# Kernel tuning notes

Hardware: AMD Instinct MI355X
Metric: run time of the kernel (lower is better)

## Reference

```python
import jax, jax.numpy as jnp
import numpy as np

B, S, D, H, HD = 2, 4096, 768, 12, 64
W = 256  # one-sided attention window (attention_window=512 // 2)
SCALE = 1.0 / np.sqrt(HD).astype(np.float32)
NEG = -1e9


def setup_inputs() -> dict:
    key = jax.random.key(0)
    ks = jax.random.split(key, 13)
    inp = {"hidden_states": jax.random.normal(ks[0], (B, S, D), dtype=jnp.float32)}
    names = ["Wq", "Wk", "Wv", "Wqg", "Wkg", "Wvg"]
    for i, n in enumerate(names):
        inp[n] = jax.random.normal(ks[1 + i], (D, D), dtype=jnp.float32) * 0.02
        inp["b" + n[1:]] = jax.random.normal(ks[7 + i], (D,), dtype=jnp.float32) * 0.02
    inp["num_global"] = 32
    return inp


def _heads(x):
    # [B,S,D] -> [B,H,S,HD]
    return x.reshape(B, S, H, HD).transpose(0, 2, 1, 3)


def longformer_attn(hidden_states, Wq, bq, Wk, bk, Wv, bv, Wqg, bqg, Wkg, bkg, Wvg, bvg, G):
    q = _heads(hidden_states @ Wq + bq) * SCALE
    k = _heads(hidden_states @ Wk + bk)
    v = _heads(hidden_states @ Wv + bv)

    nc = S // W  # number of query chunks
    # --- banded (sliding window) scores via overlapping key chunks of size 3W ---
    Qc = q.reshape(B, H, nc, W, HD)
    kpad = jnp.pad(k, ((0, 0), (0, 0), (W, W), (0, 0)))
    win_idx = jnp.arange(nc)[:, None] * W + jnp.arange(3 * W)[None, :]  # [nc, 3W]
    K3 = kpad[:, :, win_idx]  # [B,H,nc,3W,HD]
    band = jnp.einsum('bhcqd,bhckd->bhcqk', Qc, K3)  # [B,H,nc,W,3W]
    # mask: key abs position in range, and relative offset within [-W, W]
    c = jnp.arange(nc)[:, None, None]
    pq = jnp.arange(W)[None, :, None]
    e = jnp.arange(3 * W)[None, None, :]
    kabs = c * W + e - W
    valid = (kabs >= 0) & (kabs < S) & (e >= pq) & (e <= pq + 2 * W)
    band = jnp.where(valid[None, None], band, NEG).reshape(B, H, S, 3 * W)

    # --- all queries also attend to the G global keys (regular key proj) ---
    sg = jnp.einsum('bhsd,bhgd->bhsg', q, k[:, :, :G])  # [B,H,S,G]
    probs = jax.nn.softmax(jnp.concatenate([sg, band], axis=-1), axis=-1)
    pg, pb = probs[..., :G], probs[..., G:].reshape(B, H, nc, W, 3 * W)

    vpad = jnp.pad(v, ((0, 0), (0, 0), (W, W), (0, 0)))
    V3 = vpad[:, :, win_idx]  # [B,H,nc,3W,HD]
    out = jnp.einsum('bhcqk,bhckd->bhcqd', pb, V3).reshape(B, H, S, HD)
    out = out + jnp.einsum('bhsg,bhgd->bhsd', pg, v[:, :, :G])

    # --- global queries attend to ALL tokens with the *_global projections ---
    qg = _heads(hidden_states @ Wqg + bqg)[:, :, :G] * SCALE  # [B,H,G,HD]
    kgf = _heads(hidden_states @ Wkg + bkg)
    vgf = _heads(hidden_states @ Wvg + bvg)
    gp = jax.nn.softmax(jnp.einsum('bhgd,bhsd->bhgs', qg, kgf), axis=-1)
    gout = jnp.einsum('bhgs,bhsd->bhgd', gp, vgf)  # [B,H,G,HD]
    out = out.at[:, :, :G].set(gout)

    return out.transpose(0, 2, 1, 3).reshape(B, S, D)


def reference(hidden_states, Wq, bq, Wk, bk, Wv, bv, Wqg, bqg, Wkg, bkg, Wvg, bvg, num_global):
    return longformer_attn(hidden_states, Wq, bq, Wk, bk, Wv, bv, Wqg, bqg, Wkg, bkg, Wvg, bvg, int(num_global))
```

## Files before the change

### kernel.cpp

```cpp
#include <hip/hip_runtime.h>
#include <hip/hip_bf16.h>


#define DEVI __device__ __forceinline__
typedef _Float16 f16;
typedef _Float16 h4 __attribute__((ext_vector_type(4)));
typedef _Float16 f16x8 __attribute__((ext_vector_type(8)));
typedef __attribute__((ext_vector_type(4))) float float4v;

DEVI float4v mfma16(f16x8 a, f16x8 b, float4v c) {
    return __builtin_amdgcn_mfma_f32_16x16x32_f16(a, b, c, 0, 0, 0);
}

DEVI void gl_lds16(const f16* g, f16* l) {
    __builtin_amdgcn_global_load_lds(
        (const __attribute__((address_space(1))) unsigned int*)g,
        (__attribute__((address_space(3))) unsigned int*)l, 16, 0, 0);
}

__global__ __launch_bounds__(256) void prep(
    const float* __restrict__ x,
    const float* __restrict__ w0, const float* __restrict__ w1,
    const float* __restrict__ w2, const float* __restrict__ w3,
    const float* __restrict__ w4, const float* __restrict__ w5,
    f16* __restrict__ xh, f16* __restrict__ wt) {
    __shared__ float tile[64][65];
    int bid = blockIdx.x;
    if (bid < 6144) {
        int i = (bid * 256 + threadIdx.x) * 4;
        float4 v = *(const float4*)&x[i];
        h4 o = {(f16)v.x, (f16)v.y, (f16)v.z, (f16)v.w};
        *(h4*)&xh[i] = o;
    } else {
        int t = bid - 6144;
        int i = t / 144, rem = t - i * 144;
        int n0 = (rem % 12) * 64, k0 = (rem / 12) * 64;
        const float* W = (i == 0) ? w0 : (i == 1) ? w1 : (i == 2) ? w2
                       : (i == 3) ? w3 : (i == 4) ? w4 : w5;
        int tx = threadIdx.x & 63, ty = threadIdx.x >> 6;
#pragma unroll
        for (int yy = 0; yy < 64; yy += 4)
            tile[yy + ty][tx] = W[(size_t)(k0 + yy + ty) * 768 + n0 + tx];
        __syncthreads();
#pragma unroll
        for (int yy = 0; yy < 64; yy += 4)
            wt[(size_t)(i * 768 + n0 + yy + ty) * 768 + k0 + tx] = (f16)tile[tx][yy + ty];
    }
}

__global__ __launch_bounds__(256, 2) void qkv_mfma11(
    const f16* __restrict__ Xh, const f16* __restrict__ Wt,
    const float* __restrict__ b0, const float* __restrict__ b1,
    const float* __restrict__ b2, const float* __restrict__ b3,
    const float* __restrict__ b4, const float* __restrict__ b5,
    f16* __restrict__ q, f16* __restrict__ k, f16* __restrict__ vT,
    f16* __restrict__ qg, f16* __restrict__ kg, f16* __restrict__ vgT) {
    __shared__ __align__(16) char smem[73728];
    f16* As = (f16*)smem;
    f16* Bs = (f16*)(smem + 24576);
    f16* Cl = (f16*)smem;

    int tid = threadIdx.x, lane = tid & 63, wid = tid >> 6;
    int quad = lane >> 4, l15 = lane & 15;

    int L = blockIdx.x + (blockIdx.y << 6);
    int xcd = L & 7, W = L >> 3;
    int mt = xcd * 8 + (W & 7);
    int yy = W >> 3;
    int m0 = mt * 128;
    int grp = yy / 3;
    if (grp == 3 && (m0 & 4095) != 0) return;
    int nb = (yy - grp * 3) * 256;
    int wm = (wid >> 1) * 64;
    int wn = (wid & 1) * 128;
    const f16* arow0 = Xh + (size_t)m0 * 768;
    const f16* brow0 = Wt + (size_t)(grp * 768 + nb) * 768;

    float4v acc[4][8];
#pragma unroll
    for (int i = 0; i < 4; ++i)
#pragma unroll
        for (int j = 0; j < 8; ++j) acc[i][j] = (float4v){0.f, 0.f, 0.f, 0.f};

    int r0 = tid >> 2;
    int o0 = (((tid & 3) ^ ((r0 >> 1) & 3)) << 3);
    int sw8 = ((quad ^ ((l15 >> 1) & 3)) << 3);

    auto STAGE_T = [&](int kt, int buf) {
        int k0 = kt << 5;
        const f16* ag = &arow0[(size_t)r0 * 768 + k0 + o0];
        const f16* bg = &brow0[(size_t)r0 * 768 + k0 + o0];
        f16* al = As + buf * 4096 + wid * 512;
        f16* bl = Bs + buf * 8192 + wid * 512;
        gl_lds16(ag, al);
        gl_lds16(ag + (size_t)64 * 768, al + 2048);
        gl_lds16(bg, bl);
        gl_lds16(bg + (size_t)64 * 768, bl + 2048);
        gl_lds16(bg + (size_t)128 * 768, bl + 4096);
        gl_lds16(bg + (size_t)192 * 768, bl + 6144);
    };

    auto COMPUTE_T = [&](int t) {
        const f16* Ab = As + (t % 3) * 4096;
        const f16* Bb = Bs + (t % 3) * 8192;
        f16x8 af[4], bf[8];
#pragma unroll
        for (int i = 0; i < 4; ++i)
            af[i] = *(const f16x8*)&Ab[(wm + i * 16 + l15) * 32 + sw8];
#pragma unroll
        for (int j = 0; j < 8; ++j)
            bf[j] = *(const f16x8*)&Bb[(wn + j * 16 + l15) * 32 + sw8];
        __builtin_amdgcn_s_setprio(1);
#pragma unroll
        for (int i = 0; i < 4; ++i)
#pragma unroll
            for (int j = 0; j < 8; ++j)
                acc[i][j] = mfma16(af[i], bf[j], acc[i][j]);
        __builtin_amdgcn_s_setprio(0);
    };

    STAGE_T(0, 0);
    STAGE_T(1, 1);
#pragma unroll
    for (int t = 0; t < 24; ++t) {
        if (t < 23) {
            asm volatile("s_waitcnt vmcnt(6)" ::: "memory");
        } else {
            asm volatile("s_waitcnt vmcnt(0)" ::: "memory");
        }
        __builtin_amdgcn_s_barrier();
        __builtin_amdgcn_sched_barrier(0);
        if (t + 2 <= 23) STAGE_T(t + 2, (t + 2) % 3);
        COMPUTE_T(t);
    }
    __syncthreads();

    const float* Bsel = (grp == 0) ? b0 : (grp == 1) ? b1 : (grp == 2) ? b2
                      : (grp == 3) ? b3 : (grp == 4) ? b4 : b5;
    int b = m0 >> 12;
    bool tr = (grp == 2 || grp == 5);

    if (tr) {
        constexpr int CLD2 = 136;
#pragma unroll
        for (int j = 0; j < 8; ++j) {
            float bias = Bsel[nb + wn + j * 16 + l15];
#pragma unroll
            for (int i = 0; i < 4; ++i) {
                float4v a = acc[i][j];
                h4 pk = {(f16)(a[0] + bias), (f16)(a[1] + bias),
                         (f16)(a[2] + bias), (f16)(a[3] + bias)};
                *(h4*)&Cl[(wn + j * 16 + l15) * CLD2 + wm + i * 16 + quad * 4] = pk;
            }
        }
        __syncthreads();
        f16* base = (grp == 2) ? vT : vgT;
        int c = tid;
        int ncol = nb + c, h = ncol >> 6, hd = ncol & 63;
        f16* dst = &base[((size_t)((b * 12 + h) * 64 + hd)) * 4096 + (m0 & 4095)];
        const f16* src = &Cl[c * CLD2];
#pragma unroll
        for (int ii = 0; ii < 16; ++ii)
            *(f16x8*)&dst[ii * 8] = *(const f16x8*)&src[ii * 8];
    } else {
        constexpr int CLD = 264;
        float scale = (grp == 0 || grp == 3) ? 0.125f : 1.0f;
#pragma unroll
        for (int j = 0; j < 8; ++j) {
            float bias = Bsel[nb + wn + j * 16 + l15];
#pragma unroll
            for (int i = 0; i < 4; ++i) {
                float4v a = acc[i][j];
#pragma unroll
                for (int r = 0; r < 4; ++r)
                    Cl[(wm + i * 16 + quad * 4 + r) * CLD + wn + j * 16 + l15] =
                        (f16)((a[r] + bias) * scale);
            }
        }
        __syncthreads();
        int row = tid & 127, half = tid >> 7;
        int s = (m0 & 4095) + row;
        const f16* src = &Cl[row * CLD + half * 128];
        if (grp == 3) {
            if (s < 32) {
#pragma unroll
                for (int ii = 0; ii < 16; ++ii) {
                    int h = (nb >> 6) + (half << 1) + (ii >> 3), hd = (ii & 7) * 8;
                    *(f16x8*)&qg[((size_t)((b * 12 + h) * 32 + s)) * 64 + hd] =
                        *(const f16x8*)&src[ii * 8];
                }
            }
        } else {
            f16* baseb = (grp == 0) ? q : (grp == 1) ? k : kg;
#pragma unroll
            for (int ii = 0; ii < 16; ++ii) {
                int h = (nb >> 6) + (half << 1) + (ii >> 3), hd = (ii & 7) * 8;
                *(f16x8*)&baseb[((size_t)((b * 12 + h) * 4096 + s)) * 64 + hd] =
                    *(const f16x8*)&src[ii * 8];
            }
        }
    }
}

__global__ __launch_bounds__(256, 3) void band_global(
    const f16* __restrict__ q, const f16* __restrict__ k, const f16* __restrict__ vT,
    const f16* __restrict__ qg, const f16* __restrict__ kg, const f16* __restrict__ vgT,
    float* __restrict__ out, float* __restrict__ Opart, float* __restrict__ Lpart) {
    __shared__ __align__(16) char smem[51712];
    int tid = threadIdx.x, lane = tid & 63, wid = tid >> 6;
    int quad = lane >> 4, l15 = lane & 15;

    if (blockIdx.x < 768) {
        constexpr int LDK = 72, LDV = 136, LDP = 40;
        f16* Kt = (f16*)smem;
        f16* Vt = (f16*)(smem + 18432);
        f16* PW = (f16*)(smem + 35840) + wid * 32 * LDP;
        int c = blockIdx.x & 31, h = (blockIdx.x >> 5) % 12, b = blockIdx.x / 384;
        const f16* qsl = q + (size_t)(b * 12 + h) * 4096 * 64;
        const f16* ksl = k + (size_t)(b * 12 + h) * 4096 * 64;
        const f16* vsl = vT + (size_t)(b * 12 + h) * 64 * 4096;
        int q0 = c * 128;
        int pq0 = q0 + wid * 32;

        f16x8 qf[2][2];
#pragma unroll
        for (int qg2 = 0; qg2 < 2; ++qg2)
#pragma unroll
            for (int ks = 0; ks < 2; ++ks)
                qf[qg2][ks] = *(const f16x8*)&qsl[(size_t)(pq0 + qg2 * 16 + l15) * 64 +
                                                  ks * 32 + quad * 8];

        float4v Ot[4][2];
#pragma unroll
        for (int dt = 0; dt < 4; ++dt)
#pragma unroll
            for (int qg2 = 0; qg2 < 2; ++qg2) Ot[dt][qg2] = (float4v){0.f, 0.f, 0.f, 0.f};
        float lacc[2] = {0.f, 0.f};

        {
#pragma unroll
            for (int jt = 0; jt < 2; ++jt) {
                f16x8 kf0 = *(const f16x8*)&ksl[(size_t)(jt * 16 + l15) * 64 + quad * 8];
                f16x8 kf1 = *(const f16x8*)&ksl[(size_t)(jt * 16 + l15) * 64 + 32 + quad * 8];
#pragma unroll
                for (int qg2 = 0; qg2 < 2; ++qg2) {
                    float4v sacc = (float4v){0.f, 0.f, 0.f, 0.f};
                    sacc = mfma16(kf0, qf[qg2][0], sacc);
                    sacc = mfma16(kf1, qf[qg2][1], sacc);
                    float p0 = __expf(sacc[0]), p1 = __expf(sacc[1]);
                    float p2 = __expf(sacc[2]), p3 = __expf(sacc[3]);
                    lacc[qg2] += (p0 + p1) + (p2 + p3);
                    h4 pk = {(f16)p0, (f16)p1, (f16)p2, (f16)p3};
                    *(h4*)&PW[(qg2 * 16 + l15) * LDP + jt * 16 + quad * 4] = pk;
                }
            }
            f16x8 pf0 = *(const f16x8*)&PW[l15 * LDP + quad * 8];
            f16x8 pf1 = *(const f16x8*)&PW[(16 + l15) * LDP + quad * 8];
#pragma unroll
            for (int dt = 0; dt < 4; ++dt) {
                f16x8 vf = *(const f16x8*)&vsl[(size_t)(dt * 16 + l15) * 4096 + quad * 8];
                Ot[dt][0] = mfma16(vf, pf0, Ot[dt][0]);
                Ot[dt][1] = mfma16(vf, pf1, Ot[dt][1]);
            }
        }

        for (int r = 0; r < 5; ++r) {
            int kb = q0 - 256 + r * 128;
            if (kb < 0 || kb >= 4096) continue;
            __syncthreads();
            {
                int kr = tid >> 1, ko = (tid & 1) * 32;
                const f16* ks2 = &ksl[(size_t)(kb + kr) * 64 + ko];
                f16* kd = &Kt[kr * LDK + ko];
#pragma unroll
                for (int i = 0; i < 4; ++i) *(f16x8*)&kd[i * 8] = *(const f16x8*)&ks2[i * 8];
                int vr = tid >> 2, vo = (tid & 3) * 32;
                const f16* vs2 = &vsl[(size_t)vr * 4096 + kb + vo];
                f16* vd = &Vt[vr * LDV + vo];
#pragma unroll
                for (int i = 0; i < 4; ++i) *(f16x8*)&vd[i * 8] = *(const f16x8*)&vs2[i * 8];
            }
            __syncthreads();

            if (kb + 127 < pq0 - 256 || kb > pq0 + 287) continue;

#pragma unroll
            for (int tt = 0; tt < 2; ++tt) {
                int tb = kb + tt * 64;
                if (tb + 63 < pq0 - 256 || tb > pq0 + 287) continue;
#pragma unroll
                for (int hf = 0; hf < 2; ++hf) {
#pragma unroll
                    for (int jt = 0; jt < 2; ++jt) {
                        int jl = tt * 64 + hf * 32 + jt * 16;
                        f16x8 kf0 = *(const f16x8*)&Kt[(jl + l15) * LDK + quad * 8];
                        f16x8 kf1 = *(const f16x8*)&Kt[(jl + l15) * LDK + 32 + quad * 8];
                        int j0 = kb + jl;
#pragma unroll
                        for (int qg2 = 0; qg2 < 2; ++qg2) {
                            int qlo = pq0 + qg2 * 16;
                            h4 pk = {(f16)0.f, (f16)0.f, (f16)0.f, (f16)0.f};
                            bool dead = (j0 < qlo - 271) || (j0 > qlo + 271);
                            if (!dead) {
                                float4v sacc = (float4v){0.f, 0.f, 0.f, 0.f};
                                sacc = mfma16(kf0, qf[qg2][0], sacc);
                                sacc = mfma16(kf1, qf[qg2][1], sacc);
                                float p[4];
                                bool full = (j0 >= qlo - 241) && (j0 <= qlo + 241);
                                if (full) {
#pragma unroll
                                    for (int rr = 0; rr < 4; ++rr) p[rr] = __expf(sacc[rr]);
                                } else {
#pragma unroll
                                    for (int rr = 0; rr < 4; ++rr) {
                                        int d = (j0 + quad * 4 + rr) - (qlo + l15);
                                        p[rr] = ((unsigned)(d + 256) <= 512u) ? __expf(sacc[rr]) : 0.f;
                                    }
                                }
                                lacc[qg2] += (p[0] + p[1]) + (p[2] + p[3]);
                                pk = (h4){(f16)p[0], (f16)p[1], (f16)p[2], (f16)p[3]};
                            }
                            *(h4*)&PW[(qg2 * 16 + l15) * LDP + jt * 16 + quad * 4] = pk;
                        }
                    }
                    f16x8 pf0 = *(const f16x8*)&PW[l15 * LDP + quad * 8];
                    f16x8 pf1 = *(const f16x8*)&PW[(16 + l15) * LDP + quad * 8];
#pragma unroll
                    for (int dt = 0; dt < 4; ++dt) {
                        f16x8 vf = *(const f16x8*)&Vt[(dt * 16 + l15) * LDV +
                                                      tt * 64 + hf * 32 + quad * 8];
                        Ot[dt][0] = mfma16(vf, pf0, Ot[dt][0]);
                        Ot[dt][1] = mfma16(vf, pf1, Ot[dt][1]);
                    }
                }
            }
        }

#pragma unroll
        for (int qg2 = 0; qg2 < 2; ++qg2) {
            float lsum = lacc[qg2];
            lsum += __shfl_xor(lsum, 16);
            lsum += __shfl_xor(lsum, 32);
            float inv = 1.f / lsum;
            size_t orow = (size_t)(b * 4096 + pq0 + qg2 * 16 + l15) * 768 + h * 64;
#pragma unroll
            for (int dt = 0; dt < 4; ++dt) {
                float4 o4 = {Ot[dt][qg2][0] * inv, Ot[dt][qg2][1] * inv,
                             Ot[dt][qg2][2] * inv, Ot[dt][qg2][3] * inv};
                *(float4*)&out[orow + dt * 16 + quad * 4] = o4;
            }
        }
    } else {
        constexpr int LDP = 72;
        f16* PW = (f16*)smem + wid * 32 * LDP;
        float* Osh = (float*)(smem + 18432);
        float* Lsh = (float*)(smem + 18432 + 32768);
        int bid = blockIdx.x - 768;
        int sl = bid & 7, bh = bid >> 3;
        const f16* qsl = qg + (size_t)bh * 32 * 64;
        const f16* ksl = kg + (size_t)bh * 4096 * 64;
        const f16* vsl = vgT + (size_t)bh * 64 * 4096;
        int kbase = sl * 512 + wid * 128;

        f16x8 qf[2][2];
#pragma unroll
        for (int g = 0; g < 2; ++g)
#pragma unroll
            for (int ks = 0; ks < 2; ++ks)
                qf[g][ks] = *(const f16x8*)&qsl[(size_t)(g * 16 + l15) * 64 + ks * 32 + quad * 8];

        float4v Ot[4][2];
#pragma unroll
        for (int dt = 0; dt < 4; ++dt)
#pragma unroll
            for (int g = 0; g < 2; ++g) Ot[dt][g] = (float4v){0.f, 0.f, 0.f, 0.f};
        float lacc[2] = {0.f, 0.f};

#pragma unroll
        for (int hf = 0; hf < 2; ++hf) {
            int kh0 = kbase + hf * 64;
#pragma unroll
            for (int kt = 0; kt < 4; ++kt) {
                int jb = kh0 + kt * 16;
                f16x8 kf0 = *(const f16x8*)&ksl[(size_t)(jb + l15) * 64 + quad * 8];
                f16x8 kf1 = *(const f16x8*)&ksl[(size_t)(jb + l15) * 64 + 32 + quad * 8];
#pragma unroll
                for (int g = 0; g < 2; ++g) {
                    float4v sacc = (float4v){0.f, 0.f, 0.f, 0.f};
                    sacc = mfma16(kf0, qf[g][0], sacc);
                    sacc = mfma16(kf1, qf[g][1], sacc);
                    float p0 = __expf(sacc[0]), p1 = __expf(sacc[1]);
                    float p2 = __expf(sacc[2]), p3 = __expf(sacc[3]);
                    lacc[g] += (p0 + p1) + (p2 + p3);
                    h4 pk = {(f16)p0, (f16)p1, (f16)p2, (f16)p3};
                    *(h4*)&PW[(g * 16 + l15) * LDP + kt * 16 + quad * 4] = pk;
                }
            }
#pragma unroll
            for (int kh = 0; kh < 2; ++kh) {
                f16x8 pf0 = *(const f16x8*)&PW[l15 * LDP + kh * 32 + quad * 8];
                f16x8 pf1 = *(const f16x8*)&PW[(16 + l15) * LDP + kh * 32 + quad * 8];
#pragma unroll
                for (int dt = 0; dt < 4; ++dt) {
                    f16x8 vf = *(const f16x8*)&vsl[(size_t)(dt * 16 + l15) * 4096 +
                                                   kh0 + kh * 32 + quad * 8];
                    Ot[dt][0] = mfma16(vf, pf0, Ot[dt][0]);
                    Ot[dt][1] = mfma16(vf, pf1, Ot[dt][1]);
                }
            }
        }

#pragma unroll
        for (int g = 0; g < 2; ++g) {
            lacc[g] += __shfl_xor(lacc[g], 16);
            lacc[g] += __shfl_xor(lacc[g], 32);
        }
        if (quad == 0) { Lsh[wid * 32 + l15] = lacc[0]; Lsh[wid * 32 + 16 + l15] = lacc[1]; }
#pragma unroll
        for (int dt = 0; dt < 4; ++dt)
#pragma unroll
            for (int g = 0; g < 2; ++g)
#pragma unroll
                for (int r = 0; r < 4; ++r)
                    Osh[wid * 2048 + (dt * 16 + quad * 4 + r) * 32 + g * 16 + l15] = Ot[dt][g][r];
        __syncthreads();
#pragma unroll
        for (int i = 0; i < 8; ++i) {
            int idx = tid + i * 256;
            int d = idx & 63, qq = idx >> 6;
            float v = Osh[0 * 2048 + d * 32 + qq] + Osh[1 * 2048 + d * 32 + qq] +
                      Osh[2 * 2048 + d * 32 + qq] + Osh[3 * 2048 + d * 32 + qq];
            Opart[(size_t)bid * 2048 + idx] = v;
        }
        if (tid < 32)
            Lpart[bid * 32 + tid] = Lsh[0 * 32 + tid] + Lsh[1 * 32 + tid] +
                                    Lsh[2 * 32 + tid] + Lsh[3 * 32 + tid];
    }
}

__global__ __launch_bounds__(256) void global_reduce(
    const float* __restrict__ Opart, const float* __restrict__ Lpart,
    float* __restrict__ out) {
    __shared__ float Ls[32];
    int tid = threadIdx.x, bh = blockIdx.x;
    int b = bh / 12, h = bh % 12;
    if (tid < 32) {
        float s = 0.f;
#pragma unroll
        for (int sl = 0; sl < 8; ++sl) s += Lpart[(bh * 8 + sl) * 32 + tid];
        Ls[tid] = s;
    }
    __syncthreads();
#pragma unroll
    for (int i = 0; i < 8; ++i) {
        int idx = tid + i * 256;
        int d = idx & 63, qq = idx >> 6;
        float o = 0.f;
#pragma unroll
        for (int sl = 0; sl < 8; ++sl) o += Opart[(size_t)(bh * 8 + sl) * 2048 + idx];
        out[(size_t)(b * 4096 + qq) * 768 + h * 64 + d] = o / Ls[qq];
    }
}

extern "C" void kernel_launch(void* const* d_in, const int* in_sizes, int n_in,
                              void* d_out, int out_size, void* d_ws, size_t ws_size,
                              hipStream_t stream) {
    const float* hs = (const float*)d_in[0];
    float* outp = (float*)d_out;

    char* p = (char*)d_ws;
    const size_t SLAB = (size_t)2 * 12 * 4096 * 64 * sizeof(f16);
    f16* qb   = (f16*)(p + 0 * SLAB);
    f16* kb   = (f16*)(p + 1 * SLAB);
    f16* vtb  = (f16*)(p + 2 * SLAB);
    f16* kgb  = (f16*)(p + 3 * SLAB);
    f16* vgtb = (f16*)(p + 4 * SLAB);
    f16* qgb  = (f16*)(p + 5 * SLAB);
    char* p2  = p + 5 * SLAB + 196608;
    f16* xh   = (f16*)p2;
    f16* wt   = (f16*)(p2 + SLAB);
    char* p3  = p2 + SLAB + 7077888;
    float* Opart = (float*)p3;
    float* Lpart = (float*)(p3 + 1572864);

    prep<<<7008, 256, 0, stream>>>(
        hs,
        (const float*)d_in[1], (const float*)d_in[3], (const float*)d_in[5],
        (const float*)d_in[7], (const float*)d_in[9], (const float*)d_in[11],
        xh, wt);
    qkv_mfma11<<<dim3(64, 18), 256, 0, stream>>>(
        xh, wt,
        (const float*)d_in[2], (const float*)d_in[4], (const float*)d_in[6],
        (const float*)d_in[8], (const float*)d_in[10], (const float*)d_in[12],
        qb, kb, vtb, qgb, kgb, vgtb);
    band_global<<<960, 256, 0, stream>>>(
        qb, kb, vtb, qgb, kgb, vgtb, outp, Opart, Lpart);
    global_reduce<<<24, 256, 0, stream>>>(Opart, Lpart, outp);
}
```

Before: 220.8 us.

## Fuse global-query attention reduction into band kernel, drop separate reduce launch

The global-query attention for each (batch, head) now runs in a single block that loops over all 4096 keys and normalizes the result in place, instead of 192 split-K blocks that wrote partials to a separate reduction kernel. These 24 long blocks are scheduled first in the merged grid. Band blocks now skip writing the first 32 rows, which the global blocks own. This removes one kernel launch, the partial-buffer traffic and a redundant band write. The cost is less parallelism: each global block does eight times more sequential work and may become the tail of the launch.

After: 239.3 us, median of 2. 8.4% more time.

```diff
diff --git a/kernel.cpp b/kernel.cpp
--- a/kernel.cpp
+++ b/kernel.cpp
@@ -202,20 +202,107 @@
     }
 }
 
-__global__ __launch_bounds__(256, 3) void band_global(
+__global__ __launch_bounds__(256, 3) void band_global2(
     const f16* __restrict__ q, const f16* __restrict__ k, const f16* __restrict__ vT,
     const f16* __restrict__ qg, const f16* __restrict__ kg, const f16* __restrict__ vgT,
-    float* __restrict__ out, float* __restrict__ Opart, float* __restrict__ Lpart) {
+    float* __restrict__ out) {
     __shared__ __align__(16) char smem[51712];
     int tid = threadIdx.x, lane = tid & 63, wid = tid >> 6;
     int quad = lane >> 4, l15 = lane & 15;
 
-    if (blockIdx.x < 768) {
+    if (blockIdx.x < 24) {
+        constexpr int LDP = 72;
+        f16* PW = (f16*)smem + wid * 32 * LDP;
+        float* Osh = (float*)(smem + 18432);
+        float* Lsh = (float*)(smem + 18432 + 32768);
+        int bh = blockIdx.x;
+        int h = bh % 12, b = bh / 12;
+        const f16* qsl = qg + (size_t)bh * 32 * 64;
+        const f16* ksl = kg + (size_t)bh * 4096 * 64;
+        const f16* vsl = vgT + (size_t)bh * 64 * 4096;
+
+        f16x8 qf[2][2];
+#pragma unroll
+        for (int g = 0; g < 2; ++g)
+#pragma unroll
+            for (int ks = 0; ks < 2; ++ks)
+                qf[g][ks] = *(const f16x8*)&qsl[(size_t)(g * 16 + l15) * 64 + ks * 32 + quad * 8];
+
+        float4v Ot[4][2];
+#pragma unroll
+        for (int dt = 0; dt < 4; ++dt)
+#pragma unroll
+            for (int g = 0; g < 2; ++g) Ot[dt][g] = (float4v){0.f, 0.f, 0.f, 0.f};
+        float lacc[2] = {0.f, 0.f};
+
+        for (int it = 0; it < 8; ++it) {
+            int kbase = wid * 1024 + it * 128;
+#pragma unroll
+            for (int hf = 0; hf < 2; ++hf) {
+                int kh0 = kbase + hf * 64;
+#pragma unroll
+                for (int kt = 0; kt < 4; ++kt) {
+                    int jb = kh0 + kt * 16;
+                    f16x8 kf0 = *(const f16x8*)&ksl[(size_t)(jb + l15) * 64 + quad * 8];
+                    f16x8 kf1 = *(const f16x8*)&ksl[(size_t)(jb + l15) * 64 + 32 + quad * 8];
+#pragma unroll
+                    for (int g = 0; g < 2; ++g) {
+                        float4v sacc = (float4v){0.f, 0.f, 0.f, 0.f};
+                        sacc = mfma16(kf0, qf[g][0], sacc);
+                        sacc = mfma16(kf1, qf[g][1], sacc);
+                        float p0 = __expf(sacc[0]), p1 = __expf(sacc[1]);
+                        float p2 = __expf(sacc[2]), p3 = __expf(sacc[3]);
+                        lacc[g] += (p0 + p1) + (p2 + p3);
+                        h4 pk = {(f16)p0, (f16)p1, (f16)p2, (f16)p3};
+                        *(h4*)&PW[(g * 16 + l15) * LDP + kt * 16 + quad * 4] = pk;
+                    }
+                }
+#pragma unroll
+                for (int kh = 0; kh < 2; ++kh) {
+                    f16x8 pf0 = *(const f16x8*)&PW[l15 * LDP + kh * 32 + quad * 8];
+                    f16x8 pf1 = *(const f16x8*)&PW[(16 + l15) * LDP + kh * 32 + quad * 8];
+#pragma unroll
+                    for (int dt = 0; dt < 4; ++dt) {
+                        f16x8 vf = *(const f16x8*)&vsl[(size_t)(dt * 16 + l15) * 4096 +
+                                                       kh0 + kh * 32 + quad * 8];
+                        Ot[dt][0] = mfma16(vf, pf0, Ot[dt][0]);
+                        Ot[dt][1] = mfma16(vf, pf1, Ot[dt][1]);
+                    }
+                }
+            }
+        }
+
+#pragma unroll
+        for (int g = 0; g < 2; ++g) {
+            lacc[g] += __shfl_xor(lacc[g], 16);
+            lacc[g] += __shfl_xor(lacc[g], 32);
+        }
+        if (quad == 0) { Lsh[wid * 32 + l15] = lacc[0]; Lsh[wid * 32 + 16 + l15] = lacc[1]; }
+#pragma unroll
+        for (int dt = 0; dt < 4; ++dt)
+#pragma unroll
+            for (int g = 0; g < 2; ++g)
+#pragma unroll
+                for (int r = 0; r < 4; ++r)
+                    Osh[wid * 2048 + (dt * 16 + quad * 4 + r) * 32 + g * 16 + l15] = Ot[dt][g][r];
+        __syncthreads();
+#pragma unroll
+        for (int i = 0; i < 8; ++i) {
+            int idx = tid + i * 256;
+            int d = idx & 63, qq = idx >> 6;
+            float v = Osh[0 * 2048 + d * 32 + qq] + Osh[1 * 2048 + d * 32 + qq] +
+                      Osh[2 * 2048 + d * 32 + qq] + Osh[3 * 2048 + d * 32 + qq];
+            float Lq = Lsh[0 * 32 + qq] + Lsh[1 * 32 + qq] +
+                       Lsh[2 * 32 + qq] + Lsh[3 * 32 + qq];
+            out[(size_t)(b * 4096 + qq) * 768 + h * 64 + d] = v / Lq;
+        }
+    } else {
         constexpr int LDK = 72, LDV = 136, LDP = 40;
         f16* Kt = (f16*)smem;
         f16* Vt = (f16*)(smem + 18432);
         f16* PW = (f16*)(smem + 35840) + wid * 32 * LDP;
-        int c = blockIdx.x & 31, h = (blockIdx.x >> 5) % 12, b = blockIdx.x / 384;
+        int bid = blockIdx.x - 24;
+        int c = bid & 31, h = (bid >> 5) % 12, b = bid / 384;
         const f16* qsl = q + (size_t)(b * 12 + h) * 4096 * 64;
         const f16* ksl = k + (size_t)(b * 12 + h) * 4096 * 64;
         const f16* vsl = vT + (size_t)(b * 12 + h) * 64 * 4096;
@@ -336,129 +423,22 @@
             }
         }
 
-#pragma unroll
-        for (int qg2 = 0; qg2 < 2; ++qg2) {
-            float lsum = lacc[qg2];
-            lsum += __shfl_xor(lsum, 16);
-            lsum += __shfl_xor(lsum, 32);
-            float inv = 1.f / lsum;
-            size_t orow = (size_t)(b * 4096 + pq0 + qg2 * 16 + l15) * 768 + h * 64;
-#pragma unroll
-            for (int dt = 0; dt < 4; ++dt) {
-                float4 o4 = {Ot[dt][qg2][0] * inv, Ot[dt][qg2][1] * inv,
-                             Ot[dt][qg2][2] * inv, Ot[dt][qg2][3] * inv};
-                *(float4*)&out[orow + dt * 16 + quad * 4] = o4;
-            }
-        }
-    } else {
-        constexpr int LDP = 72;
-        f16* PW = (f16*)smem + wid * 32 * LDP;
-        float* Osh = (float*)(smem + 18432);
-        float* Lsh = (float*)(smem + 18432 + 32768);
-        int bid = blockIdx.x - 768;
-        int sl = bid & 7, bh = bid >> 3;
-        const f16* qsl = qg + (size_t)bh * 32 * 64;
-        const f16* ksl = kg + (size_t)bh * 4096 * 64;
-        const f16* vsl = vgT + (size_t)bh * 64 * 4096;
-        int kbase = sl * 512 + wid * 128;
-
-        f16x8 qf[2][2];
-#pragma unroll
-        for (int g = 0; g < 2; ++g)
-#pragma unroll
-            for (int ks = 0; ks < 2; ++ks)
-                qf[g][ks] = *(const f16x8*)&qsl[(size_t)(g * 16 + l15) * 64 + ks * 32 + quad * 8];
-
-        float4v Ot[4][2];
-#pragma unroll
-        for (int dt = 0; dt < 4; ++dt)
-#pragma unroll
-            for (int g = 0; g < 2; ++g) Ot[dt][g] = (float4v){0.f, 0.f, 0.f, 0.f};
-        float lacc[2] = {0.f, 0.f};
-
-#pragma unroll
-        for (int hf = 0; hf < 2; ++hf) {
-            int kh0 = kbase + hf * 64;
-#pragma unroll
-            for (int kt = 0; kt < 4; ++kt) {
-                int jb = kh0 + kt * 16;
-                f16x8 kf0 = *(const f16x8*)&ksl[(size_t)(jb + l15) * 64 + quad * 8];
-                f16x8 kf1 = *(const f16x8*)&ksl[(size_t)(jb + l15) * 64 + 32 + quad * 8];
-#pragma unroll
-                for (int g = 0; g < 2; ++g) {
-                    float4v sacc = (float4v){0.f, 0.f, 0.f, 0.f};
-                    sacc = mfma16(kf0, qf[g][0], sacc);
-                    sacc = mfma16(kf1, qf[g][1], sacc);
-                    float p0 = __expf(sacc[0]), p1 = __expf(sacc[1]);
-                    float p2 = __expf(sacc[2]), p3 = __expf(sacc[3]);
-                    lacc[g] += (p0 + p1) + (p2 + p3);
-                    h4 pk = {(f16)p0, (f16)p1, (f16)p2, (f16)p3};
-                    *(h4*)&PW[(g * 16 + l15) * LDP + kt * 16 + quad * 4] = pk;
-                }
-            }
-#pragma unroll
-            for (int kh = 0; kh < 2; ++kh) {
-                f16x8 pf0 = *(const f16x8*)&PW[l15 * LDP + kh * 32 + quad * 8];
-                f16x8 pf1 = *(const f16x8*)&PW[(16 + l15) * LDP + kh * 32 + quad * 8];
+        if (pq0 >= 32) {
+#pragma unroll
+            for (int qg2 = 0; qg2 < 2; ++qg2) {
+                float lsum = lacc[qg2];
+                lsum += __shfl_xor(lsum, 16);
+                lsum += __shfl_xor(lsum, 32);
+                float inv = 1.f / lsum;
+                size_t orow = (size_t)(b * 4096 + pq0 + qg2 * 16 + l15) * 768 + h * 64;
 #pragma unroll
                 for (int dt = 0; dt < 4; ++dt) {
-                    f16x8 vf = *(const f16x8*)&vsl[(size_t)(dt * 16 + l15) * 4096 +
-                                                   kh0 + kh * 32 + quad * 8];
-                    Ot[dt][0] = mfma16(vf, pf0, Ot[dt][0]);
-                    Ot[dt][1] = mfma16(vf, pf1, Ot[dt][1]);
-                }
-            }
-        }
-
-#pragma unroll
-        for (int g = 0; g < 2; ++g) {
-            lacc[g] += __shfl_xor(lacc[g], 16);
-            lacc[g] += __shfl_xor(lacc[g], 32);
-        }
-        if (quad == 0) { Lsh[wid * 32 + l15] = lacc[0]; Lsh[wid * 32 + 16 + l15] = lacc[1]; }
-#pragma unroll
-        for (int dt = 0; dt < 4; ++dt)
-#pragma unroll
-            for (int g = 0; g < 2; ++g)
-#pragma unroll
-                for (int r = 0; r < 4; ++r)
-                    Osh[wid * 2048 + (dt * 16 + quad * 4 + r) * 32 + g * 16 + l15] = Ot[dt][g][r];
-        __syncthreads();
-#pragma unroll
-        for (int i = 0; i < 8; ++i) {
-            int idx = tid + i * 256;
-            int d = idx & 63, qq = idx >> 6;
-            float v = Osh[0 * 2048 + d * 32 + qq] + Osh[1 * 2048 + d * 32 + qq] +
-                      Osh[2 * 2048 + d * 32 + qq] + Osh[3 * 2048 + d * 32 + qq];
-            Opart[(size_t)bid * 2048 + idx] = v;
-        }
-        if (tid < 32)
-            Lpart[bid * 32 + tid] = Lsh[0 * 32 + tid] + Lsh[1 * 32 + tid] +
-                                    Lsh[2 * 32 + tid] + Lsh[3 * 32 + tid];
-    }
-}
-
-__global__ __launch_bounds__(256) void global_reduce(
-    const float* __restrict__ Opart, const float* __restrict__ Lpart,
-    float* __restrict__ out) {
-    __shared__ float Ls[32];
-    int tid = threadIdx.x, bh = blockIdx.x;
-    int b = bh / 12, h = bh % 12;
-    if (tid < 32) {
-        float s = 0.f;
-#pragma unroll
-        for (int sl = 0; sl < 8; ++sl) s += Lpart[(bh * 8 + sl) * 32 + tid];
-        Ls[tid] = s;
-    }
-    __syncthreads();
-#pragma unroll
-    for (int i = 0; i < 8; ++i) {
-        int idx = tid + i * 256;
-        int d = idx & 63, qq = idx >> 6;
-        float o = 0.f;
-#pragma unroll
-        for (int sl = 0; sl < 8; ++sl) o += Opart[(size_t)(bh * 8 + sl) * 2048 + idx];
-        out[(size_t)(b * 4096 + qq) * 768 + h * 64 + d] = o / Ls[qq];
+                    float4 o4 = {Ot[dt][qg2][0] * inv, Ot[dt][qg2][1] * inv,
+                                 Ot[dt][qg2][2] * inv, Ot[dt][qg2][3] * inv};
+                    *(float4*)&out[orow + dt * 16 + quad * 4] = o4;
+                }
+            }
+        }
     }
 }
 
@@ -479,9 +459,6 @@
     char* p2  = p + 5 * SLAB + 196608;
     f16* xh   = (f16*)p2;
     f16* wt   = (f16*)(p2 + SLAB);
-    char* p3  = p2 + SLAB + 7077888;
-    float* Opart = (float*)p3;
-    float* Lpart = (float*)(p3 + 1572864);
 
     prep<<<7008, 256, 0, stream>>>(
         hs,
@@ -493,7 +470,6 @@
         (const float*)d_in[2], (const float*)d_in[4], (const float*)d_in[6],
         (const float*)d_in[8], (const float*)d_in[10], (const float*)d_in[12],
         qb, kb, vtb, qgb, kgb, vgtb);
-    band_global<<<960, 256, 0, stream>>>(
-        qb, kb, vtb, qgb, kgb, vgtb, outp, Opart, Lpart);
-    global_reduce<<<24, 256, 0, stream>>>(Opart, Lpart, outp);
-}
+    band_global2<<<792, 256, 0, stream>>>(
+        qb, kb, vtb, qgb, kgb, vgtb, outp);
+}
```

## Enlarge QKV GEMM tile to 256x256 with 8 waves and 4-stage split pipeline

Applied to the files above, without the earlier changes.

The fused QKV projection GEMM now uses 512-thread blocks computing 256x256 output tiles instead of 256 threads on 128x256. It uses a 4-slot LDS ring with loads issued three steps ahead, and A and B staging split across two barrier phases inside each k-step. The epilogue writes the tile in two halves so it fits the LDS scratch. This aims to raise operand reuse and hide global load latency better. In exchange it uses 128KB of LDS per block, adds extra barriers, and launches fewer blocks.

Result: slower. 232.8 us (+5.4%).

```diff
diff --git a/kernel.cpp b/kernel.cpp
--- a/kernel.cpp
+++ b/kernel.cpp
@@ -48,90 +48,105 @@
     }
 }
 
-__global__ __launch_bounds__(256, 2) void qkv_mfma11(
+__global__ __launch_bounds__(512, 2) void qkv_mfma12(
     const f16* __restrict__ Xh, const f16* __restrict__ Wt,
     const float* __restrict__ b0, const float* __restrict__ b1,
     const float* __restrict__ b2, const float* __restrict__ b3,
     const float* __restrict__ b4, const float* __restrict__ b5,
     f16* __restrict__ q, f16* __restrict__ k, f16* __restrict__ vT,
     f16* __restrict__ qg, f16* __restrict__ kg, f16* __restrict__ vgT) {
-    __shared__ __align__(16) char smem[73728];
-    f16* As = (f16*)smem;
-    f16* Bs = (f16*)(smem + 24576);
-    f16* Cl = (f16*)smem;
+    __shared__ __align__(16) char smem[131072];
+    f16* smemf = (f16*)smem;
+    f16* Cl = smemf;
 
     int tid = threadIdx.x, lane = tid & 63, wid = tid >> 6;
     int quad = lane >> 4, l15 = lane & 15;
-
-    int L = blockIdx.x + (blockIdx.y << 6);
+    int wr = wid >> 2, wc = wid & 3;
+    int wrb = wr * 128, wcb = wc * 64;
+
+    int L = blockIdx.x;
     int xcd = L & 7, W = L >> 3;
-    int mt = xcd * 8 + (W & 7);
-    int yy = W >> 3;
-    int m0 = mt * 128;
+    int mt = xcd * 4 + (W & 3);
+    int yy = W >> 2;
+    int m0 = mt * 256;
     int grp = yy / 3;
     if (grp == 3 && (m0 & 4095) != 0) return;
     int nb = (yy - grp * 3) * 256;
-    int wm = (wid >> 1) * 64;
-    int wn = (wid & 1) * 128;
     const f16* arow0 = Xh + (size_t)m0 * 768;
     const f16* brow0 = Wt + (size_t)(grp * 768 + nb) * 768;
 
-    float4v acc[4][8];
-#pragma unroll
-    for (int i = 0; i < 4; ++i)
-#pragma unroll
-        for (int j = 0; j < 8; ++j) acc[i][j] = (float4v){0.f, 0.f, 0.f, 0.f};
-
-    int r0 = tid >> 2;
-    int o0 = (((tid & 3) ^ ((r0 >> 1) & 3)) << 3);
+    float4v acc[8][4];
+#pragma unroll
+    for (int i = 0; i < 8; ++i)
+#pragma unroll
+        for (int j = 0; j < 4; ++j) acc[i][j] = (float4v){0.f, 0.f, 0.f, 0.f};
+
+    int cgl = (((lane & 3) ^ ((lane >> 3) & 3)) << 3);
     int sw8 = ((quad ^ ((l15 >> 1) & 3)) << 3);
 
-    auto STAGE_T = [&](int kt, int buf) {
+    auto Aslot = [&](int s) { return smemf + s * 16384; };
+    auto Bslot = [&](int s) { return smemf + s * 16384 + 8192; };
+    auto STAGE_A = [&](int kt, int s) {
         int k0 = kt << 5;
-        const f16* ag = &arow0[(size_t)r0 * 768 + k0 + o0];
-        const f16* bg = &brow0[(size_t)r0 * 768 + k0 + o0];
-        f16* al = As + buf * 4096 + wid * 512;
-        f16* bl = Bs + buf * 8192 + wid * 512;
-        gl_lds16(ag, al);
-        gl_lds16(ag + (size_t)64 * 768, al + 2048);
-        gl_lds16(bg, bl);
-        gl_lds16(bg + (size_t)64 * 768, bl + 2048);
-        gl_lds16(bg + (size_t)128 * 768, bl + 4096);
-        gl_lds16(bg + (size_t)192 * 768, bl + 6144);
+        const f16* g = arow0 + (size_t)(wid * 32 + (lane >> 2)) * 768 + k0 + cgl;
+        f16* l0 = Aslot(s) + (wid * 32) * 32;
+        gl_lds16(g, l0);
+        gl_lds16(g + (size_t)16 * 768, l0 + 512);
     };
-
-    auto COMPUTE_T = [&](int t) {
-        const f16* Ab = As + (t % 3) * 4096;
-        const f16* Bb = Bs + (t % 3) * 8192;
-        f16x8 af[4], bf[8];
-#pragma unroll
-        for (int i = 0; i < 4; ++i)
-            af[i] = *(const f16x8*)&Ab[(wm + i * 16 + l15) * 32 + sw8];
-#pragma unroll
-        for (int j = 0; j < 8; ++j)
-            bf[j] = *(const f16x8*)&Bb[(wn + j * 16 + l15) * 32 + sw8];
-        __builtin_amdgcn_s_setprio(1);
-#pragma unroll
-        for (int i = 0; i < 4; ++i)
-#pragma unroll
-            for (int j = 0; j < 8; ++j)
-                acc[i][j] = mfma16(af[i], bf[j], acc[i][j]);
-        __builtin_amdgcn_s_setprio(0);
+    auto STAGE_B = [&](int kt, int s) {
+        int k0 = kt << 5;
+        const f16* g = brow0 + (size_t)(wid * 32 + (lane >> 2)) * 768 + k0 + cgl;
+        f16* l0 = Bslot(s) + (wid * 32) * 32;
+        gl_lds16(g, l0);
+        gl_lds16(g + (size_t)16 * 768, l0 + 512);
     };
 
-    STAGE_T(0, 0);
-    STAGE_T(1, 1);
+    STAGE_A(0, 0); STAGE_B(0, 0);
+    STAGE_A(1, 1); STAGE_B(1, 1);
+    STAGE_A(2, 2); STAGE_B(2, 2);
 #pragma unroll
     for (int t = 0; t < 24; ++t) {
-        if (t < 23) {
-            asm volatile("s_waitcnt vmcnt(6)" ::: "memory");
-        } else {
-            asm volatile("s_waitcnt vmcnt(0)" ::: "memory");
-        }
+        if (t < 22)       asm volatile("s_waitcnt vmcnt(8)" ::: "memory");
+        else if (t == 22) asm volatile("s_waitcnt vmcnt(4)" ::: "memory");
+        else              asm volatile("s_waitcnt vmcnt(0)" ::: "memory");
         __builtin_amdgcn_s_barrier();
         __builtin_amdgcn_sched_barrier(0);
-        if (t + 2 <= 23) STAGE_T(t + 2, (t + 2) % 3);
-        COMPUTE_T(t);
+        if (t + 3 <= 23) STAGE_A(t + 3, (t + 3) & 3);
+        const f16* Ab = Aslot(t & 3);
+        const f16* Bb = Bslot(t & 3);
+        f16x8 bf[4];
+#pragma unroll
+        for (int j = 0; j < 4; ++j)
+            bf[j] = *(const f16x8*)&Bb[(wcb + j * 16 + l15) * 32 + sw8];
+        {
+            f16x8 af[4];
+#pragma unroll
+            for (int i = 0; i < 4; ++i)
+                af[i] = *(const f16x8*)&Ab[(wrb + i * 16 + l15) * 32 + sw8];
+            __builtin_amdgcn_s_setprio(1);
+#pragma unroll
+            for (int i = 0; i < 4; ++i)
+#pragma unroll
+                for (int j = 0; j < 4; ++j)
+                    acc[i][j] = mfma16(af[i], bf[j], acc[i][j]);
+            __builtin_amdgcn_s_setprio(0);
+        }
+        __builtin_amdgcn_s_barrier();
+        __builtin_amdgcn_sched_barrier(0);
+        if (t + 3 <= 23) STAGE_B(t + 3, (t + 3) & 3);
+        {
+            f16x8 af[4];
+#pragma unroll
+            for (int i = 0; i < 4; ++i)
+                af[i] = *(const f16x8*)&Ab[(wrb + 64 + i * 16 + l15) * 32 + sw8];
+            __builtin_amdgcn_s_setprio(1);
+#pragma unroll
+            for (int i = 0; i < 4; ++i)
+#pragma unroll
+                for (int j = 0; j < 4; ++j)
+                    acc[4 + i][j] = mfma16(af[i], bf[j], acc[4 + i][j]);
+            __builtin_amdgcn_s_setprio(0);
+        }
     }
     __syncthreads();
 
@@ -143,61 +158,75 @@
     if (tr) {
         constexpr int CLD2 = 136;
 #pragma unroll
-        for (int j = 0; j < 8; ++j) {
-            float bias = Bsel[nb + wn + j * 16 + l15];
-#pragma unroll
-            for (int i = 0; i < 4; ++i) {
-                float4v a = acc[i][j];
-                h4 pk = {(f16)(a[0] + bias), (f16)(a[1] + bias),
-                         (f16)(a[2] + bias), (f16)(a[3] + bias)};
-                *(h4*)&Cl[(wn + j * 16 + l15) * CLD2 + wm + i * 16 + quad * 4] = pk;
-            }
-        }
-        __syncthreads();
-        f16* base = (grp == 2) ? vT : vgT;
-        int c = tid;
-        int ncol = nb + c, h = ncol >> 6, hd = ncol & 63;
-        f16* dst = &base[((size_t)((b * 12 + h) * 64 + hd)) * 4096 + (m0 & 4095)];
-        const f16* src = &Cl[c * CLD2];
-#pragma unroll
-        for (int ii = 0; ii < 16; ++ii)
-            *(f16x8*)&dst[ii * 8] = *(const f16x8*)&src[ii * 8];
+        for (int ph = 0; ph < 2; ++ph) {
+            if (wr == ph) {
+#pragma unroll
+                for (int j = 0; j < 4; ++j) {
+                    float bias = Bsel[nb + wcb + j * 16 + l15];
+#pragma unroll
+                    for (int i = 0; i < 8; ++i) {
+                        float4v a = acc[i][j];
+                        h4 pk = {(f16)(a[0] + bias), (f16)(a[1] + bias),
+                                 (f16)(a[2] + bias), (f16)(a[3] + bias)};
+                        *(h4*)&Cl[(wcb + j * 16 + l15) * CLD2 + i * 16 + quad * 4] = pk;
+                    }
+                }
+            }
+            __syncthreads();
+            {
+                f16* base = (grp == 2) ? vT : vgT;
+                int c = tid >> 1, rh = tid & 1;
+                int ncol = nb + c, hh = ncol >> 6, hd = ncol & 63;
+                f16* dst = &base[((size_t)((b * 12 + hh) * 64 + hd)) * 4096 +
+                                 (m0 & 4095) + ph * 128 + rh * 64];
+                const f16* src = &Cl[c * CLD2 + rh * 64];
+#pragma unroll
+                for (int ii = 0; ii < 8; ++ii)
+                    *(f16x8*)&dst[ii * 8] = *(const f16x8*)&src[ii * 8];
+            }
+            __syncthreads();
+        }
     } else {
         constexpr int CLD = 264;
         float scale = (grp == 0 || grp == 3) ? 0.125f : 1.0f;
 #pragma unroll
-        for (int j = 0; j < 8; ++j) {
-            float bias = Bsel[nb + wn + j * 16 + l15];
-#pragma unroll
-            for (int i = 0; i < 4; ++i) {
-                float4v a = acc[i][j];
-#pragma unroll
-                for (int r = 0; r < 4; ++r)
-                    Cl[(wm + i * 16 + quad * 4 + r) * CLD + wn + j * 16 + l15] =
-                        (f16)((a[r] + bias) * scale);
-            }
-        }
-        __syncthreads();
-        int row = tid & 127, half = tid >> 7;
-        int s = (m0 & 4095) + row;
-        const f16* src = &Cl[row * CLD + half * 128];
-        if (grp == 3) {
-            if (s < 32) {
-#pragma unroll
-                for (int ii = 0; ii < 16; ++ii) {
-                    int h = (nb >> 6) + (half << 1) + (ii >> 3), hd = (ii & 7) * 8;
-                    *(f16x8*)&qg[((size_t)((b * 12 + h) * 32 + s)) * 64 + hd] =
-                        *(const f16x8*)&src[ii * 8];
-                }
-            }
-        } else {
-            f16* baseb = (grp == 0) ? q : (grp == 1) ? k : kg;
-#pragma unroll
-            for (int ii = 0; ii < 16; ++ii) {
-                int h = (nb >> 6) + (half << 1) + (ii >> 3), hd = (ii & 7) * 8;
-                *(f16x8*)&baseb[((size_t)((b * 12 + h) * 4096 + s)) * 64 + hd] =
-                    *(const f16x8*)&src[ii * 8];
-            }
+        for (int ph = 0; ph < 2; ++ph) {
+            if (wr == ph) {
+#pragma unroll
+                for (int j = 0; j < 4; ++j) {
+                    float bias = Bsel[nb + wcb + j * 16 + l15];
+#pragma unroll
+                    for (int i = 0; i < 8; ++i) {
+                        float4v a = acc[i][j];
+#pragma unroll
+                        for (int r = 0; r < 4; ++r)
+                            Cl[(i * 16 + quad * 4 + r) * CLD + wcb + j * 16 + l15] =
+                                (f16)((a[r] + bias) * scale);
+                    }
+                }
+            }
+            __syncthreads();
+            {
+                int row = tid & 127, qtr = tid >> 7;
+                int s = (m0 & 4095) + ph * 128 + row;
+                int hh = (nb + qtr * 64) >> 6;
+                const f16* src = &Cl[row * CLD + qtr * 64];
+                if (grp == 3) {
+                    if (s < 32) {
+                        f16* dst = &qg[((size_t)((b * 12 + hh) * 32 + s)) * 64];
+#pragma unroll
+                        for (int ii = 0; ii < 8; ++ii)
+                            *(f16x8*)&dst[ii * 8] = *(const f16x8*)&src[ii * 8];
+                    }
+                } else {
+                    f16* baseb = (grp == 0) ? q : (grp == 1) ? k : kg;
+                    f16* dst = &baseb[((size_t)((b * 12 + hh) * 4096 + s)) * 64];
+#pragma unroll
+                    for (int ii = 0; ii < 8; ++ii)
+                        *(f16x8*)&dst[ii * 8] = *(const f16x8*)&src[ii * 8];
+                }
+            }
+            __syncthreads();
         }
     }
 }
@@ -488,7 +517,7 @@
         (const float*)d_in[1], (const float*)d_in[3], (const float*)d_in[5],
         (const float*)d_in[7], (const float*)d_in[9], (const float*)d_in[11],
         xh, wt);
-    qkv_mfma11<<<dim3(64, 18), 256, 0, stream>>>(
+    qkv_mfma12<<<576, 512, 0, stream>>>(
         xh, wt,
         (const float*)d_in[2], (const float*)d_in[4], (const float*)d_in[6],
         (const float*)d_in[8], (const float*)d_in[10], (const float*)d_in[12],
```
